# Kernel optimization log

Measured on AMD Instinct MI355X. Metric: run time of the kernel, lower is better.

Reference implementation:

```python
import jax, jax.numpy as jnp
import numpy as np

P_FACTOR = 3.0
EPS = 1e-12  # torch F.normalize eps


def _l2norm(x):
    # F.normalize(x, dim=1): divide by max(||x||_2, eps) along feature dim
    n = jnp.sqrt(jnp.sum(x * x, axis=1, keepdims=True))
    return x / jnp.maximum(n, EPS)


def setup_inputs() -> dict:
    key = jax.random.key(0)
    ks = jax.random.split(key, 7)
    B, N, F, E = 4096, 20000, 768, 512
    X = jax.random.normal(ks[0], (B, F), jnp.float32)
    D = jax.random.normal(ks[1], (N, F), jnp.float32)
    r = jax.random.uniform(ks[2], (N, 1), jnp.float32)  # correctness in [0,1]
    g_w = jax.random.normal(ks[3], (E, F), jnp.float32) * (1.0 / np.sqrt(F))
    g_b = jax.random.normal(ks[4], (E,), jnp.float32) * 0.01
    h_w = jax.random.normal(ks[5], (1, 1), jnp.float32)
    h_b = jax.random.normal(ks[6], (1,), jnp.float32) * 0.01
    return {"X": X, "D": D, "r": r, "g_w": g_w, "g_b": g_b, "h_w": h_w, "h_b": h_b}


def reference(X, D, r, g_w, g_b, h_w, h_b):
    # register_buffer path: r = ex_correct * 2 - 1
    r = r * 2.0 - 1.0
    # g: Linear(feat_dim -> feat_embed_dim) on both queries and exemplars
    Xe = X @ g_w.T + g_b            # [B, E]
    De = D @ g_w.T + g_b            # [N, E]
    # h: Linear(1 -> class_embed_dim)
    rh = r @ h_w.T + h_b            # [N, C]
    # Minerva: cosine similarity -> power-law activation -> weighted retrieval
    a = _l2norm(Xe) @ _l2norm(De).T                 # [B, N]
    a = jnp.sign(a) * jnp.abs(a) ** P_FACTOR        # |s|^p * sign(s)
    logits = a @ rh                                 # [B, C]
    preds = jax.nn.sigmoid(logits)
    return logits, preds
```

## Files before the change

### kernel.cpp

```cpp
#include <hip/hip_runtime.h>
#include <cstdint>


typedef __attribute__((ext_vector_type(4))) float  f32x4;
typedef __attribute__((ext_vector_type(8))) __bf16 bf16x8;
typedef __attribute__((ext_vector_type(4))) __bf16 bf16x4;

#define AS1CAST(p) ((__attribute__((address_space(1))) unsigned int*)(uintptr_t)(p))
#define AS3CAST(p) ((__attribute__((address_space(3))) unsigned int*)(uintptr_t)(p))

__device__ __forceinline__ void gload_lds16(const void* g, void* l) {
  __builtin_amdgcn_global_load_lds(AS1CAST(g), AS3CAST(l), 16, 0, 0);
}


__global__ void k_f32_to_bf16(const float* __restrict__ in, __bf16* __restrict__ out, int n) {
  int i = (blockIdx.x * blockDim.x + threadIdx.x) * 4;
  if (i + 4 <= n) {
    float4 v = *(const float4*)(in + i);
    bf16x4 o;
    o[0] = (__bf16)v.x; o[1] = (__bf16)v.y; o[2] = (__bf16)v.z; o[3] = (__bf16)v.w;
    *(bf16x4*)(out + i) = o;
  }
}

__global__ void k_rh(const float* __restrict__ r, const float* __restrict__ hw,
                     const float* __restrict__ hb, float* __restrict__ rh, int n) {
  int i = blockIdx.x * blockDim.x + threadIdx.x;
  if (i < n) rh[i] = (2.0f * r[i] - 1.0f) * hw[0] + hb[0];
}

__global__ void k_zero_f32(float* __restrict__ p, int n) {
  int i = blockIdx.x * blockDim.x + threadIdx.x;
  if (i < n) p[i] = 0.0f;
}

__global__ void k_finalize(const float* __restrict__ logits, float* __restrict__ out, int n) {
  int i = blockIdx.x * blockDim.x + threadIdx.x;
  if (i < n) {
    float L = logits[i];
    out[i] = L;
    out[n + i] = 1.0f / (1.0f + expf(-L));
  }
}


__global__ __launch_bounds__(256, 2)
void k_embed_gemm(const __bf16* __restrict__ A, const __bf16* __restrict__ G,
                  const float* __restrict__ bias, float* __restrict__ C, int M) {
  constexpr int K = 768;
  constexpr int E = 512;
  __shared__ __bf16 As[128 * 32];
  __shared__ __bf16 Bs[128 * 32];
  const int tid  = threadIdx.x;
  const int wave = tid >> 6;
  const int lane = tid & 63;
  const int m0 = blockIdx.y * 128;
  const int n0 = blockIdx.x * 128;
  const int r_in = lane >> 2;
  const int kp   = (lane & 3) * 8;

  int ar0 = m0 + wave * 16 + r_in;        if (ar0 >= M) ar0 = M - 1;
  int ar1 = m0 + (wave + 4) * 16 + r_in;  if (ar1 >= M) ar1 = M - 1;
  const int br0 = n0 + wave * 16 + r_in;
  const int br1 = n0 + (wave + 4) * 16 + r_in;

  const __bf16* ga0 = A + (size_t)ar0 * K + kp;
  const __bf16* ga1 = A + (size_t)ar1 * K + kp;
  const __bf16* gb0 = G + (size_t)br0 * K + kp;
  const __bf16* gb1 = G + (size_t)br1 * K + kp;
  __bf16* la0 = &As[(size_t)wave * 512 + (size_t)lane * 8];
  __bf16* la1 = &As[(size_t)(wave + 4) * 512 + (size_t)lane * 8];
  __bf16* lb0 = &Bs[(size_t)wave * 512 + (size_t)lane * 8];
  __bf16* lb1 = &Bs[(size_t)(wave + 4) * 512 + (size_t)lane * 8];

  const int mw = (wave & 1) * 64;
  const int nw = (wave >> 1) * 64;
  const int quad = lane >> 4;
  const int l15  = lane & 15;

  f32x4 acc[4][4] = {};

  for (int kb = 0; kb < K; kb += 32) {
    gload_lds16(ga0 + kb, la0);
    gload_lds16(ga1 + kb, la1);
    gload_lds16(gb0 + kb, lb0);
    gload_lds16(gb1 + kb, lb1);
    __syncthreads();
    bf16x8 af[4], bfr[4];
#pragma unroll
    for (int i = 0; i < 4; ++i)
      af[i] = *(const bf16x8*)&As[(mw + i * 16 + l15) * 32 + quad * 8];
#pragma unroll
    for (int j = 0; j < 4; ++j)
      bfr[j] = *(const bf16x8*)&Bs[(nw + j * 16 + l15) * 32 + quad * 8];
#pragma unroll
    for (int i = 0; i < 4; ++i)
#pragma unroll
      for (int j = 0; j < 4; ++j)
        acc[i][j] = __builtin_amdgcn_mfma_f32_16x16x32_bf16(af[i], bfr[j], acc[i][j], 0, 0, 0);
    __syncthreads();
  }

#pragma unroll
  for (int j = 0; j < 4; ++j) {
    const int col = n0 + nw + j * 16 + l15;
    const float bv = bias[col];
#pragma unroll
    for (int i = 0; i < 4; ++i) {
      const int row = m0 + mw + i * 16 + quad * 4;
#pragma unroll
      for (int rr = 0; rr < 4; ++rr) {
        if (row + rr < M)
          C[(size_t)(row + rr) * E + col] = acc[i][j][rr] + bv;
      }
    }
  }
}


__global__ void k_normalize(const float* __restrict__ Xe, __bf16* __restrict__ Xn, int M) {
  const int row  = blockIdx.x * 4 + (threadIdx.x >> 6);
  const int lane = threadIdx.x & 63;
  if (row >= M) return;
  const float4* p = (const float4*)(Xe + (size_t)row * 512);
  float4 v0 = p[lane];
  float4 v1 = p[lane + 64];
  float s = v0.x * v0.x + v0.y * v0.y + v0.z * v0.z + v0.w * v0.w
          + v1.x * v1.x + v1.y * v1.y + v1.z * v1.z + v1.w * v1.w;
#pragma unroll
  for (int off = 32; off > 0; off >>= 1) s += __shfl_xor(s, off);
  const float sc = 1.0f / fmaxf(sqrtf(s), 1e-12f);
  bf16x4 o0, o1;
  o0[0] = (__bf16)(v0.x * sc); o0[1] = (__bf16)(v0.y * sc);
  o0[2] = (__bf16)(v0.z * sc); o0[3] = (__bf16)(v0.w * sc);
  o1[0] = (__bf16)(v1.x * sc); o1[1] = (__bf16)(v1.y * sc);
  o1[2] = (__bf16)(v1.z * sc); o1[3] = (__bf16)(v1.w * sc);
  bf16x4* q = (bf16x4*)(Xn + (size_t)row * 512);
  q[lane]      = o0;
  q[lane + 64] = o1;
}


__global__ __launch_bounds__(256, 2)
void k_minerva(const __bf16* __restrict__ Xn, const __bf16* __restrict__ Dn,
               const float* __restrict__ rh, float* __restrict__ logits, int N) {
  constexpr int K = 512;
  __shared__ __bf16 As[128 * 32];
  __shared__ __bf16 Bs[128 * 32];
  __shared__ float lsum[128];
  const int tid  = threadIdx.x;
  const int wave = tid >> 6;
  const int lane = tid & 63;
  const int m0 = blockIdx.y * 128;
  const int n0 = blockIdx.x * 128;
  if (tid < 128) lsum[tid] = 0.0f;

  const int r_in = lane >> 2;
  const int kp   = (lane & 3) * 8;

  const int ar0 = m0 + wave * 16 + r_in;
  const int ar1 = m0 + (wave + 4) * 16 + r_in;
  int br0 = n0 + wave * 16 + r_in;        if (br0 >= N) br0 = N - 1;
  int br1 = n0 + (wave + 4) * 16 + r_in;  if (br1 >= N) br1 = N - 1;

  const __bf16* ga0 = Xn + (size_t)ar0 * K + kp;
  const __bf16* ga1 = Xn + (size_t)ar1 * K + kp;
  const __bf16* gb0 = Dn + (size_t)br0 * K + kp;
  const __bf16* gb1 = Dn + (size_t)br1 * K + kp;
  __bf16* la0 = &As[(size_t)wave * 512 + (size_t)lane * 8];
  __bf16* la1 = &As[(size_t)(wave + 4) * 512 + (size_t)lane * 8];
  __bf16* lb0 = &Bs[(size_t)wave * 512 + (size_t)lane * 8];
  __bf16* lb1 = &Bs[(size_t)(wave + 4) * 512 + (size_t)lane * 8];

  const int mw = (wave & 1) * 64;
  const int nw = (wave >> 1) * 64;
  const int quad = lane >> 4;
  const int l15  = lane & 15;

  f32x4 acc[4][4] = {};

  for (int kb = 0; kb < K; kb += 32) {
    gload_lds16(ga0 + kb, la0);
    gload_lds16(ga1 + kb, la1);
    gload_lds16(gb0 + kb, lb0);
    gload_lds16(gb1 + kb, lb1);
    __syncthreads();
    bf16x8 af[4], bfr[4];
#pragma unroll
    for (int i = 0; i < 4; ++i)
      af[i] = *(const bf16x8*)&As[(mw + i * 16 + l15) * 32 + quad * 8];
#pragma unroll
    for (int j = 0; j < 4; ++j)
      bfr[j] = *(const bf16x8*)&Bs[(nw + j * 16 + l15) * 32 + quad * 8];
#pragma unroll
    for (int i = 0; i < 4; ++i)
#pragma unroll
      for (int j = 0; j < 4; ++j)
        acc[i][j] = __builtin_amdgcn_mfma_f32_16x16x32_bf16(af[i], bfr[j], acc[i][j], 0, 0, 0);
    __syncthreads();
  }

  float rhv[4];
#pragma unroll
  for (int j = 0; j < 4; ++j) {
    const int col = n0 + nw + j * 16 + l15;
    rhv[j] = (col < N) ? rh[col] : 0.0f;
  }
#pragma unroll
  for (int i = 0; i < 4; ++i) {
    float part[4] = {0.0f, 0.0f, 0.0f, 0.0f};
#pragma unroll
    for (int j = 0; j < 4; ++j)
#pragma unroll
      for (int rr = 0; rr < 4; ++rr) {
        const float s = acc[i][j][rr];
        part[rr] += s * s * s * rhv[j];
      }
#pragma unroll
    for (int rr = 0; rr < 4; ++rr) {
      float v = part[rr];
      v += __shfl_xor(v, 1);
      v += __shfl_xor(v, 2);
      v += __shfl_xor(v, 4);
      v += __shfl_xor(v, 8);
      if (l15 == 0) atomicAdd(&lsum[mw + i * 16 + quad * 4 + rr], v);
    }
  }
  __syncthreads();
  if (tid < 128) atomicAdd(&logits[m0 + tid], lsum[tid]);
}


extern "C" void kernel_launch(void* const* d_in, const int* in_sizes, int n_in,
                              void* d_out, int out_size, void* d_ws, size_t ws_size,
                              hipStream_t stream) {
  constexpr int B = 4096, N = 20000, F = 768, E = 512;

  const float* X   = (const float*)d_in[0];
  const float* D   = (const float*)d_in[1];
  const float* r   = (const float*)d_in[2];
  const float* g_w = (const float*)d_in[3];
  const float* g_b = (const float*)d_in[4];
  const float* h_w = (const float*)d_in[5];
  const float* h_b = (const float*)d_in[6];
  float* out = (float*)d_out;

  char* ws = (char*)d_ws;
  __bf16* Xb  = (__bf16*)(ws + 0);
  __bf16* Db  = (__bf16*)(ws + 6291456);
  __bf16* Gb  = (__bf16*)(ws + 37011456);
  float*  Xe  = (float*) (ws + 37797888);
  float*  De  = (float*) (ws + 46186496);
  __bf16* Xn  = (__bf16*)(ws + 87146496);
  __bf16* Dn  = (__bf16*)(ws + 91340800);
  float*  rh  = (float*) (ws + 111820800);
  float*  lg  = (float*) (ws + 111900800);

  k_f32_to_bf16<<<(B * F / 4 + 255) / 256, 256, 0, stream>>>(X, Xb, B * F);
  k_f32_to_bf16<<<(N * F / 4 + 255) / 256, 256, 0, stream>>>(D, Db, N * F);
  k_f32_to_bf16<<<(E * F / 4 + 255) / 256, 256, 0, stream>>>(g_w, Gb, E * F);
  k_rh<<<(N + 255) / 256, 256, 0, stream>>>(r, h_w, h_b, rh, N);

  k_embed_gemm<<<dim3(E / 128, B / 128), 256, 0, stream>>>(Xb, Gb, g_b, Xe, B);
  k_embed_gemm<<<dim3(E / 128, (N + 127) / 128), 256, 0, stream>>>(Db, Gb, g_b, De, N);

  k_normalize<<<B / 4, 256, 0, stream>>>(Xe, Xn, B);
  k_normalize<<<N / 4, 256, 0, stream>>>(De, Dn, N);

  k_zero_f32<<<(B + 255) / 256, 256, 0, stream>>>(lg, B);
  k_minerva<<<dim3((N + 127) / 128, B / 128), 256, 0, stream>>>(Xn, Dn, rh, lg, N);

  k_finalize<<<(B + 255) / 256, 256, 0, stream>>>(lg, out, B);
}
```

Baseline: 314.2 us.

## Fuse prep and embed kernels, fold norms into GEMM epilogue, swizzle Minerva tiles

Merges the three fp32-to-bf16 conversions, the rh computation and the buffer zeroing into a single grid-stride prep kernel. The X and D embedding GEMMs now run as one launch that writes bf16 embeddings and accumulates squared row norms in the epilogue, instead of writing fp32 and re-reading it. Normalization then only scales the bf16 embeddings by the precomputed norms. The similarity GEMM moves to a K-step of 64 with an XOR-swizzled LDS layout to avoid bank conflicts, and uses a panelled block order for better L2 reuse of D tiles. Together these cut launches and intermediate memory traffic, at the cost of computing norms from bf16-rounded values and using float atomics for the norm sums.

```diff
diff --git a/kernel.cpp b/kernel.cpp
--- a/kernel.cpp
+++ b/kernel.cpp
@@ -6,6 +6,8 @@
 typedef __attribute__((ext_vector_type(8))) __bf16 bf16x8;
 typedef __attribute__((ext_vector_type(4))) __bf16 bf16x4;
 
+constexpr int B = 4096, N = 20000, F = 768, E = 512;
+
 #define AS1CAST(p) ((__attribute__((address_space(1))) unsigned int*)(uintptr_t)(p))
 #define AS3CAST(p) ((__attribute__((address_space(3))) unsigned int*)(uintptr_t)(p))
 
@@ -14,61 +16,63 @@
 }
 
 
-__global__ void k_f32_to_bf16(const float* __restrict__ in, __bf16* __restrict__ out, int n) {
-  int i = (blockIdx.x * blockDim.x + threadIdx.x) * 4;
-  if (i + 4 <= n) {
-    float4 v = *(const float4*)(in + i);
+__global__ void k_prep(const float* __restrict__ X, const float* __restrict__ D,
+                       const float* __restrict__ G, const float* __restrict__ r,
+                       const float* __restrict__ hw, const float* __restrict__ hb,
+                       __bf16* __restrict__ Xb, __bf16* __restrict__ Db,
+                       __bf16* __restrict__ Gb, float* __restrict__ rh,
+                       float* __restrict__ lg, float* __restrict__ norm2) {
+  const int t = blockIdx.x * blockDim.x + threadIdx.x;
+  const int stride = gridDim.x * blockDim.x;
+  constexpr int nX = B * F / 4, nD = N * F / 4, nG = E * F / 4;
+  constexpr int tot = nX + nD + nG;
+  for (int i = t; i < tot; i += stride) {
+    const float4* src; bf16x4* dst; int off;
+    if (i < nX)           { src = (const float4*)X; dst = (bf16x4*)Xb; off = i; }
+    else if (i < nX + nD) { src = (const float4*)D; dst = (bf16x4*)Db; off = i - nX; }
+    else                  { src = (const float4*)G; dst = (bf16x4*)Gb; off = i - nX - nD; }
+    float4 v = src[off];
     bf16x4 o;
     o[0] = (__bf16)v.x; o[1] = (__bf16)v.y; o[2] = (__bf16)v.z; o[3] = (__bf16)v.w;
-    *(bf16x4*)(out + i) = o;
-  }
-}
-
-__global__ void k_rh(const float* __restrict__ r, const float* __restrict__ hw,
-                     const float* __restrict__ hb, float* __restrict__ rh, int n) {
-  int i = blockIdx.x * blockDim.x + threadIdx.x;
-  if (i < n) rh[i] = (2.0f * r[i] - 1.0f) * hw[0] + hb[0];
-}
-
-__global__ void k_zero_f32(float* __restrict__ p, int n) {
-  int i = blockIdx.x * blockDim.x + threadIdx.x;
-  if (i < n) p[i] = 0.0f;
-}
-
-__global__ void k_finalize(const float* __restrict__ logits, float* __restrict__ out, int n) {
-  int i = blockIdx.x * blockDim.x + threadIdx.x;
-  if (i < n) {
-    float L = logits[i];
-    out[i] = L;
-    out[n + i] = 1.0f / (1.0f + expf(-L));
-  }
+    dst[off] = o;
+  }
+  if (t < N) rh[t] = (2.0f * r[t] - 1.0f) * hw[0] + hb[0];
+  if (t < B) lg[t] = 0.0f;
+  if (t < B + N) norm2[t] = 0.0f;
 }
 
 
 __global__ __launch_bounds__(256, 2)
-void k_embed_gemm(const __bf16* __restrict__ A, const __bf16* __restrict__ G,
-                  const float* __restrict__ bias, float* __restrict__ C, int M) {
-  constexpr int K = 768;
-  constexpr int E = 512;
+void k_embed(const __bf16* __restrict__ Xb, const __bf16* __restrict__ Db,
+             const __bf16* __restrict__ Gb, const float* __restrict__ bias,
+             __bf16* __restrict__ Eb, float* __restrict__ norm2) {
+  constexpr int K = F;
   __shared__ __bf16 As[128 * 32];
   __shared__ __bf16 Bs[128 * 32];
+  __shared__ float ssum[128];
   const int tid  = threadIdx.x;
   const int wave = tid >> 6;
   const int lane = tid & 63;
-  const int m0 = blockIdx.y * 128;
+  const int by = blockIdx.y;
+  const bool isX = (by < B / 128);
+  const __bf16* A = isX ? Xb : Db;
+  const int m0 = isX ? by * 128 : (by - B / 128) * 128;
+  const int Mr = isX ? B : N;
+  const int g0 = by * 128;
   const int n0 = blockIdx.x * 128;
+  if (tid < 128) ssum[tid] = 0.0f;
+
   const int r_in = lane >> 2;
   const int kp   = (lane & 3) * 8;
-
-  int ar0 = m0 + wave * 16 + r_in;        if (ar0 >= M) ar0 = M - 1;
-  int ar1 = m0 + (wave + 4) * 16 + r_in;  if (ar1 >= M) ar1 = M - 1;
+  int ar0 = m0 + wave * 16 + r_in;        if (ar0 >= Mr) ar0 = Mr - 1;
+  int ar1 = m0 + (wave + 4) * 16 + r_in;  if (ar1 >= Mr) ar1 = Mr - 1;
   const int br0 = n0 + wave * 16 + r_in;
   const int br1 = n0 + (wave + 4) * 16 + r_in;
 
   const __bf16* ga0 = A + (size_t)ar0 * K + kp;
   const __bf16* ga1 = A + (size_t)ar1 * K + kp;
-  const __bf16* gb0 = G + (size_t)br0 * K + kp;
-  const __bf16* gb1 = G + (size_t)br1 * K + kp;
+  const __bf16* gb0 = Gb + (size_t)br0 * K + kp;
+  const __bf16* gb1 = Gb + (size_t)br1 * K + kp;
   __bf16* la0 = &As[(size_t)wave * 512 + (size_t)lane * 8];
   __bf16* la1 = &As[(size_t)(wave + 4) * 512 + (size_t)lane * 8];
   __bf16* lb0 = &Bs[(size_t)wave * 512 + (size_t)lane * 8];
@@ -103,101 +107,124 @@
   }
 
 #pragma unroll
-  for (int j = 0; j < 4; ++j) {
-    const int col = n0 + nw + j * 16 + l15;
-    const float bv = bias[col];
-#pragma unroll
-    for (int i = 0; i < 4; ++i) {
-      const int row = m0 + mw + i * 16 + quad * 4;
+  for (int i = 0; i < 4; ++i) {
+    float part[4] = {0.0f, 0.0f, 0.0f, 0.0f};
+#pragma unroll
+    for (int j = 0; j < 4; ++j) {
+      const int col = n0 + nw + j * 16 + l15;
+      const float bv = bias[col];
 #pragma unroll
       for (int rr = 0; rr < 4; ++rr) {
-        if (row + rr < M)
-          C[(size_t)(row + rr) * E + col] = acc[i][j][rr] + bv;
+        const int row = mw + i * 16 + quad * 4 + rr;
+        if (m0 + row < Mr) {
+          const __bf16 hv = (__bf16)(acc[i][j][rr] + bv);
+          Eb[(size_t)(g0 + row) * E + col] = hv;
+          const float vb = (float)hv;
+          part[rr] += vb * vb;
+        }
       }
     }
-  }
-}
-
-
-__global__ void k_normalize(const float* __restrict__ Xe, __bf16* __restrict__ Xn, int M) {
+#pragma unroll
+    for (int rr = 0; rr < 4; ++rr) {
+      float v = part[rr];
+      v += __shfl_xor(v, 1);
+      v += __shfl_xor(v, 2);
+      v += __shfl_xor(v, 4);
+      v += __shfl_xor(v, 8);
+      if (l15 == 0) atomicAdd(&ssum[mw + i * 16 + quad * 4 + rr], v);
+    }
+  }
+  __syncthreads();
+  if (tid < 128 && m0 + tid < Mr) atomicAdd(&norm2[g0 + tid], ssum[tid]);
+}
+
+
+__global__ void k_normall(const __bf16* __restrict__ Eb, const float* __restrict__ norm2,
+                          __bf16* __restrict__ Nb, int rows) {
   const int row  = blockIdx.x * 4 + (threadIdx.x >> 6);
   const int lane = threadIdx.x & 63;
-  if (row >= M) return;
-  const float4* p = (const float4*)(Xe + (size_t)row * 512);
-  float4 v0 = p[lane];
-  float4 v1 = p[lane + 64];
-  float s = v0.x * v0.x + v0.y * v0.y + v0.z * v0.z + v0.w * v0.w
-          + v1.x * v1.x + v1.y * v1.y + v1.z * v1.z + v1.w * v1.w;
-#pragma unroll
-  for (int off = 32; off > 0; off >>= 1) s += __shfl_xor(s, off);
-  const float sc = 1.0f / fmaxf(sqrtf(s), 1e-12f);
-  bf16x4 o0, o1;
-  o0[0] = (__bf16)(v0.x * sc); o0[1] = (__bf16)(v0.y * sc);
-  o0[2] = (__bf16)(v0.z * sc); o0[3] = (__bf16)(v0.w * sc);
-  o1[0] = (__bf16)(v1.x * sc); o1[1] = (__bf16)(v1.y * sc);
-  o1[2] = (__bf16)(v1.z * sc); o1[3] = (__bf16)(v1.w * sc);
-  bf16x4* q = (bf16x4*)(Xn + (size_t)row * 512);
-  q[lane]      = o0;
-  q[lane + 64] = o1;
+  if (row >= rows) return;
+  bf16x8 v = ((const bf16x8*)(Eb + (size_t)row * E))[lane];
+  const float sc = 1.0f / fmaxf(sqrtf(norm2[row]), 1e-12f);
+  bf16x8 o;
+#pragma unroll
+  for (int k = 0; k < 8; ++k) o[k] = (__bf16)((float)v[k] * sc);
+  ((bf16x8*)(Nb + (size_t)row * E))[lane] = o;
 }
 
 
 __global__ __launch_bounds__(256, 2)
 void k_minerva(const __bf16* __restrict__ Xn, const __bf16* __restrict__ Dn,
-               const float* __restrict__ rh, float* __restrict__ logits, int N) {
-  constexpr int K = 512;
-  __shared__ __bf16 As[128 * 32];
-  __shared__ __bf16 Bs[128 * 32];
+               const float* __restrict__ rh, float* __restrict__ logits) {
+  constexpr int K  = 512;
+  constexpr int MT = B / 128;
+  constexpr int NT = (N + 127) / 128;
+  constexpr int W  = 20;
+  __shared__ __bf16 As[128 * 64];
+  __shared__ __bf16 Bs[128 * 64];
   __shared__ float lsum[128];
   const int tid  = threadIdx.x;
+  const int lane = tid & 63;
   const int wave = tid >> 6;
-  const int lane = tid & 63;
-  const int m0 = blockIdx.y * 128;
-  const int n0 = blockIdx.x * 128;
+
+  const int bid   = blockIdx.x;
+  const int panel = bid / (W * MT);
+  const int bn    = panel * W;
+  const int Wp    = min(W, NT - bn);
+  const int rem   = bid - panel * (W * MT);
+  const int mt    = rem / Wp;
+  const int nt    = bn + rem % Wp;
+  const int m0 = mt * 128, n0 = nt * 128;
   if (tid < 128) lsum[tid] = 0.0f;
 
-  const int r_in = lane >> 2;
-  const int kp   = (lane & 3) * 8;
-
-  const int ar0 = m0 + wave * 16 + r_in;
-  const int ar1 = m0 + (wave + 4) * 16 + r_in;
-  int br0 = n0 + wave * 16 + r_in;        if (br0 >= N) br0 = N - 1;
-  int br1 = n0 + (wave + 4) * 16 + r_in;  if (br1 >= N) br1 = N - 1;
-
-  const __bf16* ga0 = Xn + (size_t)ar0 * K + kp;
-  const __bf16* ga1 = Xn + (size_t)ar1 * K + kp;
-  const __bf16* gb0 = Dn + (size_t)br0 * K + kp;
-  const __bf16* gb1 = Dn + (size_t)br1 * K + kp;
-  __bf16* la0 = &As[(size_t)wave * 512 + (size_t)lane * 8];
-  __bf16* la1 = &As[(size_t)(wave + 4) * 512 + (size_t)lane * 8];
-  __bf16* lb0 = &Bs[(size_t)wave * 512 + (size_t)lane * 8];
-  __bf16* lb1 = &Bs[(size_t)(wave + 4) * 512 + (size_t)lane * 8];
+  const int srow = tid >> 3;
+  const int scg  = (tid & 7) ^ (srow & 7);
+  const __bf16* ga[4];
+  const __bf16* gb[4];
+  __bf16* la[4];
+  __bf16* lb[4];
+#pragma unroll
+  for (int q = 0; q < 4; ++q) {
+    const int row = srow + q * 32;
+    const int arow = m0 + row;
+    int brow = n0 + row; if (brow >= N) brow = N - 1;
+    ga[q] = Xn + (size_t)arow * K + scg * 8;
+    gb[q] = Dn + (size_t)brow * K + scg * 8;
+    la[q] = &As[q * 2048 + tid * 8];
+    lb[q] = &Bs[q * 2048 + tid * 8];
+  }
 
   const int mw = (wave & 1) * 64;
   const int nw = (wave >> 1) * 64;
   const int quad = lane >> 4;
   const int l15  = lane & 15;
-
   f32x4 acc[4][4] = {};
 
-  for (int kb = 0; kb < K; kb += 32) {
-    gload_lds16(ga0 + kb, la0);
-    gload_lds16(ga1 + kb, la1);
-    gload_lds16(gb0 + kb, lb0);
-    gload_lds16(gb1 + kb, lb1);
+  for (int kb = 0; kb < K; kb += 64) {
+#pragma unroll
+    for (int q = 0; q < 4; ++q) gload_lds16(ga[q] + kb, la[q]);
+#pragma unroll
+    for (int q = 0; q < 4; ++q) gload_lds16(gb[q] + kb, lb[q]);
     __syncthreads();
-    bf16x8 af[4], bfr[4];
-#pragma unroll
-    for (int i = 0; i < 4; ++i)
-      af[i] = *(const bf16x8*)&As[(mw + i * 16 + l15) * 32 + quad * 8];
-#pragma unroll
-    for (int j = 0; j < 4; ++j)
-      bfr[j] = *(const bf16x8*)&Bs[(nw + j * 16 + l15) * 32 + quad * 8];
-#pragma unroll
-    for (int i = 0; i < 4; ++i)
-#pragma unroll
-      for (int j = 0; j < 4; ++j)
-        acc[i][j] = __builtin_amdgcn_mfma_f32_16x16x32_bf16(af[i], bfr[j], acc[i][j], 0, 0, 0);
+#pragma unroll
+    for (int h = 0; h < 2; ++h) {
+      bf16x8 af[4], bfr[4];
+#pragma unroll
+      for (int i = 0; i < 4; ++i) {
+        const int r = mw + i * 16 + l15;
+        af[i] = *(const bf16x8*)&As[r * 64 + ((quad + h * 4) ^ (r & 7)) * 8];
+      }
+#pragma unroll
+      for (int j = 0; j < 4; ++j) {
+        const int r = nw + j * 16 + l15;
+        bfr[j] = *(const bf16x8*)&Bs[r * 64 + ((quad + h * 4) ^ (r & 7)) * 8];
+      }
+#pragma unroll
+      for (int i = 0; i < 4; ++i)
+#pragma unroll
+        for (int j = 0; j < 4; ++j)
+          acc[i][j] = __builtin_amdgcn_mfma_f32_16x16x32_bf16(af[i], bfr[j], acc[i][j], 0, 0, 0);
+    }
     __syncthreads();
   }
 
@@ -232,11 +259,19 @@
 }
 
 
+__global__ void k_finalize(const float* __restrict__ logits, float* __restrict__ out, int n) {
+  int i = blockIdx.x * blockDim.x + threadIdx.x;
+  if (i < n) {
+    float L = logits[i];
+    out[i] = L;
+    out[n + i] = 1.0f / (1.0f + expf(-L));
+  }
+}
+
+
 extern "C" void kernel_launch(void* const* d_in, const int* in_sizes, int n_in,
                               void* d_out, int out_size, void* d_ws, size_t ws_size,
                               hipStream_t stream) {
-  constexpr int B = 4096, N = 20000, F = 768, E = 512;
-
   const float* X   = (const float*)d_in[0];
   const float* D   = (const float*)d_in[1];
   const float* r   = (const float*)d_in[2];
@@ -247,29 +282,23 @@
   float* out = (float*)d_out;
 
   char* ws = (char*)d_ws;
-  __bf16* Xb  = (__bf16*)(ws + 0);
-  __bf16* Db  = (__bf16*)(ws + 6291456);
-  __bf16* Gb  = (__bf16*)(ws + 37011456);
-  float*  Xe  = (float*) (ws + 37797888);
-  float*  De  = (float*) (ws + 46186496);
-  __bf16* Xn  = (__bf16*)(ws + 87146496);
-  __bf16* Dn  = (__bf16*)(ws + 91340800);
-  float*  rh  = (float*) (ws + 111820800);
-  float*  lg  = (float*) (ws + 111900800);
-
-  k_f32_to_bf16<<<(B * F / 4 + 255) / 256, 256, 0, stream>>>(X, Xb, B * F);
-  k_f32_to_bf16<<<(N * F / 4 + 255) / 256, 256, 0, stream>>>(D, Db, N * F);
-  k_f32_to_bf16<<<(E * F / 4 + 255) / 256, 256, 0, stream>>>(g_w, Gb, E * F);
-  k_rh<<<(N + 255) / 256, 256, 0, stream>>>(r, h_w, h_b, rh, N);
-
-  k_embed_gemm<<<dim3(E / 128, B / 128), 256, 0, stream>>>(Xb, Gb, g_b, Xe, B);
-  k_embed_gemm<<<dim3(E / 128, (N + 127) / 128), 256, 0, stream>>>(Db, Gb, g_b, De, N);
-
-  k_normalize<<<B / 4, 256, 0, stream>>>(Xe, Xn, B);
-  k_normalize<<<N / 4, 256, 0, stream>>>(De, Dn, N);
-
-  k_zero_f32<<<(B + 255) / 256, 256, 0, stream>>>(lg, B);
-  k_minerva<<<dim3((N + 127) / 128, B / 128), 256, 0, stream>>>(Xn, Dn, rh, lg, N);
+  __bf16* Xb    = (__bf16*)(ws + 0);
+  __bf16* Db    = (__bf16*)(ws + 6291456);
+  __bf16* Gb    = (__bf16*)(ws + 37011456);
+  __bf16* Eb    = (__bf16*)(ws + 37797888);
+  __bf16* Nb    = (__bf16*)(ws + 62472192);
+  float*  rh    = (float*) (ws + 87146496);
+  float*  norm2 = (float*) (ws + 87226496);
+  float*  lg    = (float*) (ws + 87322880);
+
+  k_prep<<<2048, 256, 0, stream>>>(X, D, g_w, r, h_w, h_b, Xb, Db, Gb, rh, lg, norm2);
+
+  k_embed<<<dim3(E / 128, B / 128 + (N + 127) / 128), 256, 0, stream>>>(
+      Xb, Db, Gb, g_b, Eb, norm2);
+
+  k_normall<<<(B + N + 3) / 4, 256, 0, stream>>>(Eb, norm2, Nb, B + N);
+
+  k_minerva<<<7 * 20 * 32 + 17 * 32, 256, 0, stream>>>(Nb, Nb + (size_t)B * E, rh, lg);
 
   k_finalize<<<(B + 255) / 256, 256, 0, stream>>>(lg, out, B);
 }
```

After: 258.7 us. 1.21x faster.
